# Optimization experiments

Hardware: AMD Instinct MI355X
Metric: run time of the kernel (lower is better)

The kernel has to match this reference:

```python
import jax, jax.numpy as jnp
import numpy as np


def gelu(x):
    # custom GELU classes in such repos typically implement the tanh approximation
    return jax.nn.gelu(x, approximate=True)


def setup_inputs() -> dict:
    key = jax.random.key(0)
    ks = jax.random.split(key, 16)
    B, N1, N2, D, H = 4, 1024, 1024, 256, 4
    prev = jax.random.normal(ks[0], (B, N1, D), dtype=jnp.float32)
    curr = jax.random.normal(ks[1], (B, N2, D), dtype=jnp.float32)
    edges = jax.random.randint(ks[2], (B, N1, N2), 0, 2).astype(jnp.int32)

    def lin(k, fan_in, fan_out):
        kw, kb = jax.random.split(k)
        s = 1.0 / np.sqrt(fan_in)
        W = jax.random.uniform(kw, (fan_in, fan_out), jnp.float32, -s, s)
        b = jax.random.uniform(kb, (fan_out,), jnp.float32, -s, s)
        return W, b

    W_pre, b_pre = lin(ks[3], D, 6)
    W_cur, b_cur = lin(ks[4], D, 6)
    W_fuse, b_fuse = lin(ks[5], 12, 4)
    W_ffn, b_ffn = lin(ks[6], 12, 8)
    W_fcc, b_fcc = lin(ks[7], 8, H)
    W_fcg, b_fcg = lin(ks[8], 8, D)
    return {"prev": prev, "curr": curr, "edges": edges,
            "W_pre": W_pre, "b_pre": b_pre, "W_cur": W_cur, "b_cur": b_cur,
            "W_fuse": W_fuse, "b_fuse": b_fuse, "W_ffn": W_ffn, "b_ffn": b_ffn,
            "W_fcc": W_fcc, "b_fcc": b_fcc, "W_fcg": W_fcg, "b_fcg": b_fcg}


def reference(prev, curr, edges, W_pre, b_pre, W_cur, b_cur,
              W_fuse, b_fuse, W_ffn, b_ffn, W_fcc, b_fcc, W_fcg, b_fcg):
    B, N1, D = prev.shape
    N2 = curr.shape[1]
    H = W_fcc.shape[1]
    Dh = D // H
    mask = edges != 0                                   # [B,N1,N2]

    bt_pre = prev @ W_pre + b_pre                       # [B,N1,6]
    bt_cur = curr @ W_cur + b_cur                       # [B,N2,6]
    pair = jnp.concatenate([
        jnp.broadcast_to(bt_pre[:, :, None, :], (B, N1, N2, 6)),
        jnp.broadcast_to(bt_cur[:, None, :, :], (B, N1, N2, 6))], axis=-1)
    c = gelu(pair) @ W_fuse + b_fuse                    # [B,N1,N2,4]
    c = jnp.where(mask[..., None], c, 0.0)

    e1 = (jnp.sum(edges, axis=1) + 1).astype(c.dtype)   # [B,N2]
    d = jnp.sum(c, axis=1)[:, None] / e1[:, None, :, None]
    d = jnp.broadcast_to(d, c.shape)
    e = jnp.broadcast_to(jnp.max(c, axis=1)[:, None], c.shape)
    fused = gelu(jnp.concatenate([c, d, e], axis=-1)) @ W_ffn + b_ffn  # [B,N1,N2,8]

    att = gelu(fused) @ W_fcc + b_fcc                   # [B,N1,N2,H]
    att = jnp.transpose(att, (0, 2, 1, 3))              # [B,N2,N1,H]
    maskT = jnp.transpose(mask, (0, 2, 1))              # [B,N2,N1]
    logits = jnp.where(maskT[..., None], att, -9e15)
    p = jax.nn.softmax(logits, axis=2)                  # softmax over N1 per head
    p = jnp.where(maskT[..., None], p, 0.0)
    # per-head aggregation: head i uses prev columns [i*Dh, (i+1)*Dh)
    res = jnp.einsum('bmnh,bnhd->bmhd', p, prev.reshape(B, N1, H, Dh)).reshape(B, N2, D)

    fused_m = jnp.where(mask[..., None], fused, 0.0)
    g = jnp.sum(fused_m, axis=1) / e1[..., None]        # [B,N2,8]
    return res + gelu(g) @ W_fcg + b_fcg                # [B,N2,D]
```

## Files before the change

kernel.cpp:

```cpp
#include <hip/hip_runtime.h>


using bf16x8 = __attribute__((ext_vector_type(8))) short;
using f32x4  = __attribute__((ext_vector_type(4))) float;
typedef float v2f __attribute__((ext_vector_type(2)));

__device__ __forceinline__ v2f pk_fma(v2f a, v2f b, v2f c){
    return __builtin_elementwise_fma(a, b, c);
}

__device__ __forceinline__ float gelu_f(float x){
    float x2 = x*x;
    float tt = x * __builtin_fmaf(0.044715f, x2, 1.0f);
    float e  = exp2f(-2.3022082f * tt);
    return x * __builtin_amdgcn_rcpf(1.0f + e);
}

__device__ __forceinline__ v2f gelu2(v2f x){
    v2f x2 = x*x;
    v2f tt = x * pk_fma((v2f){0.044715f,0.044715f}, x2, (v2f){1.0f,1.0f});
    float e0 = exp2f(-2.3022082f * tt[0]);
    float e1 = exp2f(-2.3022082f * tt[1]);
    v2f r = { __builtin_amdgcn_rcpf(1.0f + e0),
              __builtin_amdgcn_rcpf(1.0f + e1) };
    return x * r;
}

__device__ __forceinline__ unsigned short f2bf(float f){
    unsigned int u = __float_as_uint(f);
    u += 0x7FFFu + ((u >> 16) & 1u);
    return (unsigned short)(u >> 16);
}

__global__ __launch_bounds__(256) void k_rowsT(
    const float* __restrict__ prev, const float* __restrict__ curr,
    const float* __restrict__ W_pre, const float* __restrict__ b_pre,
    const float* __restrict__ W_cur, const float* __restrict__ b_cur,
    const float* __restrict__ W_fuse, const float* __restrict__ b_fuse,
    float* __restrict__ u_ws, float* __restrict__ v_ws,
    unsigned short* __restrict__ prevT)
{
    __shared__ float tile[64][65];
    int t = threadIdx.x;
    if (blockIdx.x < 2048){
        int gid  = blockIdx.x * 256 + t;
        int wave = gid >> 6;
        int lane = t & 63;
        bool isPrev = wave < 4096;
        int row = isPrev ? wave : (wave - 4096);
        const float* xrow = (isPrev ? prev : curr) + (size_t)row * 256;
        const float* W  = isPrev ? W_pre : W_cur;
        const float* bv = isPrev ? b_pre : b_cur;

        float4 x4 = *reinterpret_cast<const float4*>(xrow + lane*4);
        const float* Wl = W + lane*24;
        float p[6];
        #pragma unroll
        for (int k=0;k<6;++k)
            p[k] = x4.x*Wl[k] + x4.y*Wl[6+k] + x4.z*Wl[12+k] + x4.w*Wl[18+k];
        #pragma unroll
        for (int off=32; off>=1; off>>=1){
            #pragma unroll
            for (int k=0;k<6;++k) p[k] += __shfl_xor(p[k], off, 64);
        }
        if (lane == 0){
            float g[6];
            #pragma unroll
            for(int k=0;k<6;++k) g[k] = gelu_f(p[k] + bv[k]);
            int rb = isPrev ? 0 : 6;
            float o[4];
            #pragma unroll
            for(int kk=0;kk<4;++kk){
                float a = isPrev ? 0.0f : b_fuse[kk];
                #pragma unroll
                for(int k=0;k<6;++k) a += g[k]*W_fuse[(rb+k)*4+kk];
                o[kk]=a;
            }
            float* dst = (isPrev ? u_ws : v_ws) + (size_t)row*4;
            *reinterpret_cast<float4*>(dst) = make_float4(o[0],o[1],o[2],o[3]);
        }
    } else {
        int pbid = blockIdx.x - 2048;
        int b  = pbid >> 6;
        int it = (pbid >> 2) & 15;
        int dt = pbid & 3;
        int i0 = it*64, d0 = dt*64;
        int col = t & 63, rw = t >> 6;
        #pragma unroll
        for (int r = 0; r < 16; ++r){
            int row = rw + 4*r;
            tile[row][col] = prev[((size_t)b*1024 + i0 + row)*256 + d0 + col];
        }
        __syncthreads();
        #pragma unroll
        for (int r = 0; r < 16; ++r){
            int drow = rw + 4*r;
            prevT[((size_t)b*256 + d0 + drow)*1024 + i0 + col]
                = f2bf(tile[col][drow]);
        }
    }
}

__global__ __launch_bounds__(256) void k_cols(
    const int* __restrict__ edges,
    const float* __restrict__ u_ws, const float* __restrict__ v_ws,
    const float* __restrict__ W_ffn, const float* __restrict__ b_ffn,
    float* __restrict__ Gd_ws, float* __restrict__ cnt_ws)
{
    int b  = blockIdx.x >> 6;
    int j0 = (blockIdx.x & 63) * 16;
    int t  = threadIdx.x;
    int jq = t & 3, sl = t >> 2;
    const int*   eb = edges + (size_t)b*1048576 + j0 + jq*4;
    const float* ub = u_ws + (size_t)b*4096;

    int   cnt[4] = {0,0,0,0};
    float S[4][4] = {{0.f}};
    float M[4][4];
    #pragma unroll
    for (int q=0;q<4;++q)
        #pragma unroll
        for (int k=0;k<4;++k) M[q][k] = -3.4e38f;

    #pragma unroll 4
    for (int ii=0; ii<16; ++ii){
        int i = sl*16 + ii;
        int4   e4 = *reinterpret_cast<const int4*>(eb + (size_t)i*1024);
        float4 u4 = *reinterpret_cast<const float4*>(ub + i*4);
        float uu[4] = {u4.x,u4.y,u4.z,u4.w};
        int   ee[4] = {e4.x,e4.y,e4.z,e4.w};
        #pragma unroll
        for (int q=0;q<4;++q){
            bool mk = ee[q]!=0;
            cnt[q] += mk ? 1 : 0;
            #pragma unroll
            for (int k=0;k<4;++k){
                S[q][k] += mk ? uu[k] : 0.0f;
                M[q][k]  = mk ? fmaxf(M[q][k],uu[k]) : M[q][k];
            }
        }
    }
    __shared__ float rS[64][16][4];
    __shared__ float rM[64][16][4];
    __shared__ int   rC[64][16];
    #pragma unroll
    for (int q=0;q<4;++q){
        int c = jq*4+q;
        #pragma unroll
        for (int k=0;k<4;++k){ rS[sl][c][k]=S[q][k]; rM[sl][c][k]=M[q][k]; }
        rC[sl][c]=cnt[q];
    }
    __syncthreads();
    float aS[4], aM[4]; int aC=0; int c2=0, hf=0;
    if (t < 128){
        c2 = t & 15; hf = t >> 4;
        #pragma unroll
        for(int k=0;k<4;++k){ aS[k]=0.f; aM[k]=-3.4e38f; }
        for (int s2=hf*8; s2<hf*8+8; ++s2){
            aC += rC[s2][c2];
            #pragma unroll
            for(int k=0;k<4;++k){ aS[k]+=rS[s2][c2][k]; aM[k]=fmaxf(aM[k],rM[s2][c2][k]); }
        }
    }
    __syncthreads();
    if (t < 128){
        rC[hf][c2]=aC;
        #pragma unroll
        for(int k=0;k<4;++k){ rS[hf][c2][k]=aS[k]; rM[hf][c2][k]=aM[k]; }
    }
    __syncthreads();
    if (t < 16){
        int cc=0; float Sa[4]={0,0,0,0};
        float Ma[4]={-3.4e38f,-3.4e38f,-3.4e38f,-3.4e38f};
        for (int s2=0;s2<8;++s2){
            cc += rC[s2][t];
            #pragma unroll
            for(int k=0;k<4;++k){ Sa[k]+=rS[s2][t][k]; Ma[k]=fmaxf(Ma[k],rM[s2][t][k]); }
        }
        size_t cj = (size_t)b*1024 + j0 + t;
        float4 v4 = *reinterpret_cast<const float4*>(v_ws + cj*4);
        float vv[4]={v4.x,v4.y,v4.z,v4.w};
        float cf = (float)cc, e1 = cf + 1.0f;
        float gd[4], ge[4];
        #pragma unroll
        for(int k=0;k<4;++k){
            float dk = (Sa[k] + cf*vv[k]) / e1;
            float ek;
            if (cc == 0) ek = 0.0f;
            else { float m1 = Ma[k]+vv[k]; ek = (cc < 1024) ? fmaxf(m1, 0.0f) : m1; }
            gd[k]=gelu_f(dk); ge[k]=gelu_f(ek);
        }
        #pragma unroll
        for(int kk=0;kk<8;++kk){
            float a = b_ffn[kk];
            #pragma unroll
            for(int k=0;k<4;++k)
                a += gd[k]*W_ffn[(4+k)*8+kk] + ge[k]*W_ffn[(8+k)*8+kk];
            Gd_ws[cj*8+kk]=a;
        }
        cnt_ws[cj]=cf;
    }
}

template<int SPLIT>
__global__ __launch_bounds__(256) void k_main(
    const unsigned short* __restrict__ prevT, const int* __restrict__ edges,
    const float* __restrict__ u_ws, const float* __restrict__ v_ws,
    const float* __restrict__ Gd_ws,
    const float* __restrict__ W_ffn, const float* __restrict__ W_fcc,
    const float* __restrict__ b_fcc,
    float* __restrict__ Pws, float* __restrict__ Sws, float* __restrict__ Tws)
{
    const int RPB = 1024/SPLIT;
    int bid = blockIdx.x;
    int sp  = bid & (SPLIT-1);
    int jt  = (bid / SPLIT) & 63;
    int b   = bid / (SPLIT*64);
    int j0  = jt*16;
    int t   = threadIdx.x;
    int lane = t & 63;
    int wv   = t >> 6;
    int jl_w = t & 15, il_w = t >> 4;

    __shared__ unsigned short wA[2][4096];
    __shared__ __align__(16) float sU[2][64][4];
    __shared__ float sV[16][4];
    __shared__ float sGd[16][8];

    if (t < 64)  (&sV[0][0])[t]  = v_ws[((size_t)b*1024 + j0)*4 + t];
    if (t < 128) (&sGd[0][0])[t] = Gd_ws[((size_t)b*1024 + j0)*8 + t];

    const float LOG2E = 1.4426950408889634f;
    v2f W4p[4][4], Wfcp[8][2], bfcp[2];
    #pragma unroll
    for(int k=0;k<4;++k)
        #pragma unroll
        for(int q=0;q<4;++q)
            W4p[k][q] = (v2f){W_ffn[k*8+2*q], W_ffn[k*8+2*q+1]};
    #pragma unroll
    for(int kk=0;kk<8;++kk)
        #pragma unroll
        for(int p2=0;p2<2;++p2)
            Wfcp[kk][p2] = (v2f){W_fcc[kk*4+2*p2]*LOG2E, W_fcc[kk*4+2*p2+1]*LOG2E};
    #pragma unroll
    for(int p2=0;p2<2;++p2)
        bfcp[p2] = (v2f){b_fcc[2*p2]*LOG2E, b_fcc[2*p2+1]*LOG2E};

    f32x4 accm[4];
    #pragma unroll
    for (int tile=0;tile<4;++tile) accm[tile] = (f32x4){0.f,0.f,0.f,0.f};
    f32x4 accs = (f32x4){0.f,0.f,0.f,0.f};
    bf16x8 onesB;
    #pragma unroll
    for (int e=0;e<8;++e) onesB[e] = (short)0x3F80;
    v2f Tp01 = {0,0}, Tp23 = {0,0};

    const int* ebase = edges + (size_t)b*1048576 + j0;
    const int NCH = RPB/64;
    const int base_i0 = sp*RPB;

    int arow = lane & 15, kgrp = lane >> 4;
    int aoff0 = (((wv*16 + arow)*64 + kgrp*8)*2) ^ ((arow & 7) << 4);
    int aoff1 = aoff0 ^ 64;
    const unsigned short* pTbase = prevT
        + ((size_t)b*256 + wv*64 + arow)*1024 + base_i0 + kgrp*8;

    float su_r = u_ws[((size_t)b*1024 + base_i0)*4 + t];
    (&sU[0][0][0])[t] = su_r;
    int egr[4];
    #pragma unroll
    for (int r=0;r<4;++r)
        egr[r] = ebase[(size_t)(base_i0 + il_w + 16*r)*1024 + jl_w];
    {
        int i0n = base_i0 + ((1 < NCH) ? 64 : 0);
        su_r = u_ws[((size_t)b*1024 + i0n)*4 + t];
    }
    __syncthreads();

    float4 v4p = *reinterpret_cast<const float4*>(&sV[jl_w][0]);
    float4 gd0 = *reinterpret_cast<const float4*>(&sGd[jl_w][0]);
    float4 gd1 = *reinterpret_cast<const float4*>(&sGd[jl_w][4]);

    for (int cc=0; cc<NCH; ++cc){
        int p = cc & 1;
        char* wAp = reinterpret_cast<char*>(wA) + p*8192;

        int eg_c[4] = {egr[0], egr[1], egr[2], egr[3]};
        {
            int i0n = base_i0 + ((cc+1 < NCH) ? (cc+1)*64 : 0);
            #pragma unroll
            for (int r=0;r<4;++r)
                egr[r] = ebase[(size_t)(i0n + il_w + 16*r)*1024 + jl_w];
        }

        #pragma unroll
        for (int r=0;r<4;++r){
            int il = il_w + 16*r;
            int eg = eg_c[r];
            float4 u4 = *reinterpret_cast<const float4*>(&sU[p][il][0]);
            v2f g01 = gelu2((v2f){u4.x + v4p.x, u4.y + v4p.y});
            v2f g23 = gelu2((v2f){u4.z + v4p.z, u4.w + v4p.w});
            float m = eg ? 1.0f : 0.0f;
            v2f mm = {m, m};
            Tp01 = pk_fma(mm, g01, Tp01);
            Tp23 = pk_fma(mm, g23, Tp23);
            v2f a0 = {gd0.x, gd0.y}, a1 = {gd0.z, gd0.w};
            v2f a2 = {gd1.x, gd1.y}, a3 = {gd1.z, gd1.w};
            v2f G0 = {g01[0], g01[0]}, G1 = {g01[1], g01[1]};
            v2f G2 = {g23[0], g23[0]}, G3 = {g23[1], g23[1]};
            a0 = pk_fma(G0, W4p[0][0], a0); a1 = pk_fma(G0, W4p[0][1], a1);
            a2 = pk_fma(G0, W4p[0][2], a2); a3 = pk_fma(G0, W4p[0][3], a3);
            a0 = pk_fma(G1, W4p[1][0], a0); a1 = pk_fma(G1, W4p[1][1], a1);
            a2 = pk_fma(G1, W4p[1][2], a2); a3 = pk_fma(G1, W4p[1][3], a3);
            a0 = pk_fma(G2, W4p[2][0], a0); a1 = pk_fma(G2, W4p[2][1], a1);
            a2 = pk_fma(G2, W4p[2][2], a2); a3 = pk_fma(G2, W4p[2][3], a3);
            a0 = pk_fma(G3, W4p[3][0], a0); a1 = pk_fma(G3, W4p[3][1], a1);
            a2 = pk_fma(G3, W4p[3][2], a2); a3 = pk_fma(G3, W4p[3][3], a3);
            v2f f01 = gelu2(a0), f23 = gelu2(a1);
            v2f f45 = gelu2(a2), f67 = gelu2(a3);
            v2f L01 = bfcp[0], L23 = bfcp[1];
            float fv[8] = {f01[0],f01[1],f23[0],f23[1],f45[0],f45[1],f67[0],f67[1]};
            #pragma unroll
            for (int kk=0;kk<8;++kk){
                v2f F = {fv[kk], fv[kk]};
                L01 = pk_fma(F, Wfcp[kk][0], L01);
                L23 = pk_fma(F, Wfcp[kk][1], L23);
            }
            float lg[4] = {L01[0], L01[1], L23[0], L23[1]};
            int low = ((jl_w*64 + il)*2) ^ ((jl_w & 7) << 4);
            #pragma unroll
            for (int hh=0;hh<4;++hh){
                float wf = eg ? exp2f(lg[hh]) : 0.0f;
                *reinterpret_cast<unsigned short*>(wAp + hh*2048 + low) = f2bf(wf);
            }
        }

        (&sU[p^1][0][0])[t] = su_r;
        {
            int i0n2 = base_i0 + ((cc+2 < NCH) ? (cc+2)*64 : 0);
            su_r = u_ws[((size_t)b*1024 + i0n2)*4 + t];
        }
        __syncthreads();

        bf16x8 afr0 = *reinterpret_cast<const bf16x8*>(wAp + aoff0);
        bf16x8 afr1 = *reinterpret_cast<const bf16x8*>(wAp + aoff1);
        const unsigned short* pT = pTbase + (size_t)cc*64;
        #pragma unroll
        for (int tile=0; tile<4; ++tile){
            const unsigned short* pB = pT + (size_t)tile*16*1024;
            bf16x8 bfr0 = *reinterpret_cast<const bf16x8*>(pB);
            bf16x8 bfr1 = *reinterpret_cast<const bf16x8*>(pB + 32);
            accm[tile] = __builtin_amdgcn_mfma_f32_16x16x32_bf16(
                afr0, bfr0, accm[tile], 0, 0, 0);
            accm[tile] = __builtin_amdgcn_mfma_f32_16x16x32_bf16(
                afr1, bfr1, accm[tile], 0, 0, 0);
        }
        accs = __builtin_amdgcn_mfma_f32_16x16x32_bf16(afr0, onesB, accs, 0,0,0);
        accs = __builtin_amdgcn_mfma_f32_16x16x32_bf16(afr1, onesB, accs, 0,0,0);
    }

    size_t bp = ((size_t)b*64 + jt)*SPLIT + sp;

    float* sT4 = reinterpret_cast<float*>(wA);
    {
        float* ts = sT4 + (size_t)t*4;
        ts[0]=Tp01[0]; ts[1]=Tp01[1]; ts[2]=Tp23[0]; ts[3]=Tp23[1];
    }
    __syncthreads();
    if (t < 16){
        float T0=0,T1=0,T2=0,T3=0;
        for (int s2=0;s2<16;++s2){
            const float* p = sT4 + (size_t)(s2*16 + t)*4;
            T0+=p[0]; T1+=p[1]; T2+=p[2]; T3+=p[3];
        }
        float* td = Tws + (bp*16 + t)*4;
        td[0]=T0; td[1]=T1; td[2]=T2; td[3]=T3;
    }

    if (arow == 0){
        #pragma unroll
        for (int r2=0; r2<4; ++r2)
            Sws[bp*64 + wv*16 + kgrp*4 + r2] = accs[r2];
    }
    {
        #pragma unroll
        for (int tile=0; tile<4; ++tile){
            #pragma unroll
            for (int r2=0; r2<4; ++r2){
                int j   = kgrp*4 + r2;
                int dim = wv*64 + tile*16 + arow;
                Pws[((size_t)bp*16 + j)*256 + dim] = accm[tile][r2];
            }
        }
    }
}

template<int SPLIT>
__global__ __launch_bounds__(256) void k_merge(
    const float* __restrict__ Pws, const float* __restrict__ Sws,
    const float* __restrict__ Tws,
    const float* __restrict__ Gd_ws, const float* __restrict__ cnt_ws,
    const float* __restrict__ W_ffn, const float* __restrict__ W_fcg,
    const float* __restrict__ b_fcg, float* __restrict__ out)
{
    int b   = blockIdx.x >> 7;
    int jt8 = blockIdx.x & 127;
    int jt16 = jt8 >> 1;
    int cb  = (jt8 & 1) * 8;
    int j0  = jt8*8;
    int t  = threadIdx.x;
    int jl = t >> 5, hd = t & 31, h = hd >> 3, dq = hd & 7;
    int col = cb + jl;
    __shared__ float sG[8][8];

    size_t bp0 = ((size_t)b*64 + jt16)*SPLIT;
    float s = 0.0f, acc[8] = {0,0,0,0,0,0,0,0};
    #pragma unroll
    for (int sp2=0; sp2<SPLIT; ++sp2){
        const float* p = Pws + ((bp0+sp2)*16 + col)*256 + hd*8;
        float4 p0 = *reinterpret_cast<const float4*>(p);
        float4 p1 = *reinterpret_cast<const float4*>(p+4);
        acc[0]+=p0.x; acc[1]+=p0.y; acc[2]+=p0.z; acc[3]+=p0.w;
        acc[4]+=p1.x; acc[5]+=p1.y; acc[6]+=p1.z; acc[7]+=p1.w;
        s += Sws[(bp0+sp2)*64 + h*16 + col];
    }
    if (t < 8){
        float T[4] = {0,0,0,0};
        #pragma unroll
        for (int sp2=0; sp2<SPLIT; ++sp2){
            const float* tp = Tws + ((bp0+sp2)*16 + cb + t)*4;
            #pragma unroll
            for (int k=0;k<4;++k) T[k]+=tp[k];
        }
        size_t cj = (size_t)b*1024 + j0 + t;
        float cf = cnt_ws[cj];
        float inv = __fdividef(1.0f, cf + 1.0f);
        #pragma unroll
        for (int kk=0;kk<8;++kk){
            float a = cf*Gd_ws[cj*8+kk];
            #pragma unroll
            for (int k=0;k<4;++k) a += T[k]*W_ffn[k*8+kk];
            sG[t][kk] = gelu_f(a*inv);
        }
    }
    __syncthreads();

    float rs = (s > 0.0f) ? (1.0f/s) : 0.0f;
    int col0 = h*64 + dq*8;
    float gg[8];
    #pragma unroll
    for (int kk=0;kk<8;++kk) gg[kk]=sG[jl][kk];
    float o[8];
    #pragma unroll
    for (int d2=0;d2<8;++d2){
        float a = b_fcg[col0+d2];
        #pragma unroll
        for (int kk=0;kk<8;++kk) a += gg[kk]*W_fcg[kk*256 + col0 + d2];
        o[d2] = acc[d2]*rs + a;
    }
    float* ob = out + ((size_t)b*1024 + j0 + jl)*256 + col0;
    float4* o4 = reinterpret_cast<float4*>(ob);
    o4[0] = make_float4(o[0],o[1],o[2],o[3]);
    o4[1] = make_float4(o[4],o[5],o[6],o[7]);
}

extern "C" void kernel_launch(void* const* d_in, const int* in_sizes, int n_in,
                              void* d_out, int out_size, void* d_ws, size_t ws_size,
                              hipStream_t stream)
{
    const float* prev  = (const float*)d_in[0];
    const float* curr  = (const float*)d_in[1];
    const int*   edges = (const int*)  d_in[2];
    const float* W_pre = (const float*)d_in[3];
    const float* b_pre = (const float*)d_in[4];
    const float* W_cur = (const float*)d_in[5];
    const float* b_cur = (const float*)d_in[6];
    const float* W_fuse= (const float*)d_in[7];
    const float* b_fuse= (const float*)d_in[8];
    const float* W_ffn = (const float*)d_in[9];
    const float* b_ffn = (const float*)d_in[10];
    const float* W_fcc = (const float*)d_in[11];
    const float* b_fcc = (const float*)d_in[12];
    const float* W_fcg = (const float*)d_in[13];
    const float* b_fcg = (const float*)d_in[14];
    float* out = (float*)d_out;

    float* u_ws   = (float*)d_ws;
    float* v_ws   = u_ws  + 16384;
    float* Gd_ws  = v_ws  + 16384;
    float* cnt_ws = Gd_ws + 32768;
    float* Pws    = cnt_ws + 4096;
    const size_t base_f = 16384 + 16384 + 32768 + 4096;

    const size_t p4  = (size_t)1024*16*256;
    const size_t s4v = (size_t)1024*64;
    const size_t t4  = (size_t)1024*16*4;
    const size_t pT_f = (size_t)4*256*1024/2;
    const size_t need4 = (base_f + p4 + s4v + t4 + pT_f) * 4;
    const size_t p2 = p4/2, s2v = s4v/2, t2 = t4/2;
    const size_t need2 = (base_f + p2 + s2v + t2 + pT_f) * 4;
    const size_t p1 = p4/4, s1 = s4v/4, t1 = t4/4;

    if (ws_size >= need4){
        float* Sws = Pws + p4;
        float* Tws = Sws + s4v;
        unsigned short* prevT = (unsigned short*)(Tws + t4);
        k_rowsT<<<dim3(2304), dim3(256), 0, stream>>>(prev, curr, W_pre, b_pre,
            W_cur, b_cur, W_fuse, b_fuse, u_ws, v_ws, prevT);
        k_cols<<<dim3(256), dim3(256), 0, stream>>>(edges, u_ws, v_ws,
            W_ffn, b_ffn, Gd_ws, cnt_ws);
        k_main<4><<<dim3(1024), dim3(256), 0, stream>>>(prevT, edges, u_ws,
            v_ws, Gd_ws, W_ffn, W_fcc, b_fcc, Pws, Sws, Tws);
        k_merge<4><<<dim3(512), dim3(256), 0, stream>>>(Pws, Sws, Tws, Gd_ws,
            cnt_ws, W_ffn, W_fcg, b_fcg, out);
    } else if (ws_size >= need2){
        float* Sws = Pws + p2;
        float* Tws = Sws + s2v;
        unsigned short* prevT = (unsigned short*)(Tws + t2);
        k_rowsT<<<dim3(2304), dim3(256), 0, stream>>>(prev, curr, W_pre, b_pre,
            W_cur, b_cur, W_fuse, b_fuse, u_ws, v_ws, prevT);
        k_cols<<<dim3(256), dim3(256), 0, stream>>>(edges, u_ws, v_ws,
            W_ffn, b_ffn, Gd_ws, cnt_ws);
        k_main<2><<<dim3(512), dim3(256), 0, stream>>>(prevT, edges, u_ws,
            v_ws, Gd_ws, W_ffn, W_fcc, b_fcc, Pws, Sws, Tws);
        k_merge<2><<<dim3(512), dim3(256), 0, stream>>>(Pws, Sws, Tws, Gd_ws,
            cnt_ws, W_ffn, W_fcg, b_fcg, out);
    } else {
        float* Sws = Pws + p1;
        float* Tws = Sws + s1;
        unsigned short* prevT = (unsigned short*)(Tws + t1);
        k_rowsT<<<dim3(2304), dim3(256), 0, stream>>>(prev, curr, W_pre, b_pre,
            W_cur, b_cur, W_fuse, b_fuse, u_ws, v_ws, prevT);
        k_cols<<<dim3(256), dim3(256), 0, stream>>>(edges, u_ws, v_ws,
            W_ffn, b_ffn, Gd_ws, cnt_ws);
        k_main<1><<<dim3(256), dim3(256), 0, stream>>>(prevT, edges, u_ws,
            v_ws, Gd_ws, W_ffn, W_fcc, b_fcc, Pws, Sws, Tws);
        k_merge<1><<<dim3(512), dim3(256), 0, stream>>>(Pws, Sws, Tws, Gd_ws,
            cnt_ws, W_ffn, W_fcg, b_fcg, out);
    }
}
```

Measured before the change: 69.61 us.

## Split main kernel's reduction rows eight ways and single-buffer shared staging

Adds an eight-way split over the N1 reduction dimension of the main attention kernel, which doubles the grid to 2048 blocks, when the workspace is large enough. The shared-memory double buffers for the weight tile and u rows become single buffers, with an extra barrier per chunk. The aim is more parallelism and lower LDS use per block, so occupancy can rise. The cost is more partial results for the merge kernel to reduce, half as many chunks per block, and an added sync point that serialises the staging step. The SPLIT=1 fallback path is removed.

```diff
diff --git a/kernel.cpp b/kernel.cpp
--- a/kernel.cpp
+++ b/kernel.cpp
@@ -222,8 +222,8 @@
     int wv   = t >> 6;
     int jl_w = t & 15, il_w = t >> 4;
 
-    __shared__ unsigned short wA[2][4096];
-    __shared__ __align__(16) float sU[2][64][4];
+    __shared__ unsigned short wA[4096];
+    __shared__ __align__(16) float sU[64][4];
     __shared__ float sV[16][4];
     __shared__ float sGd[16][8];
 
@@ -266,15 +266,10 @@
         + ((size_t)b*256 + wv*64 + arow)*1024 + base_i0 + kgrp*8;
 
     float su_r = u_ws[((size_t)b*1024 + base_i0)*4 + t];
-    (&sU[0][0][0])[t] = su_r;
     int egr[4];
     #pragma unroll
     for (int r=0;r<4;++r)
         egr[r] = ebase[(size_t)(base_i0 + il_w + 16*r)*1024 + jl_w];
-    {
-        int i0n = base_i0 + ((1 < NCH) ? 64 : 0);
-        su_r = u_ws[((size_t)b*1024 + i0n)*4 + t];
-    }
     __syncthreads();
 
     float4 v4p = *reinterpret_cast<const float4*>(&sV[jl_w][0]);
@@ -282,12 +277,13 @@
     float4 gd1 = *reinterpret_cast<const float4*>(&sGd[jl_w][4]);
 
     for (int cc=0; cc<NCH; ++cc){
-        int p = cc & 1;
-        char* wAp = reinterpret_cast<char*>(wA) + p*8192;
+        (&sU[0][0])[t] = su_r;
+        __syncthreads();
 
         int eg_c[4] = {egr[0], egr[1], egr[2], egr[3]};
         {
             int i0n = base_i0 + ((cc+1 < NCH) ? (cc+1)*64 : 0);
+            su_r = u_ws[((size_t)b*1024 + i0n)*4 + t];
             #pragma unroll
             for (int r=0;r<4;++r)
                 egr[r] = ebase[(size_t)(i0n + il_w + 16*r)*1024 + jl_w];
@@ -297,7 +293,7 @@
         for (int r=0;r<4;++r){
             int il = il_w + 16*r;
             int eg = eg_c[r];
-            float4 u4 = *reinterpret_cast<const float4*>(&sU[p][il][0]);
+            float4 u4 = *reinterpret_cast<const float4*>(&sU[il][0]);
             v2f g01 = gelu2((v2f){u4.x + v4p.x, u4.y + v4p.y});
             v2f g23 = gelu2((v2f){u4.z + v4p.z, u4.w + v4p.w});
             float m = eg ? 1.0f : 0.0f;
@@ -331,19 +327,16 @@
             #pragma unroll
             for (int hh=0;hh<4;++hh){
                 float wf = eg ? exp2f(lg[hh]) : 0.0f;
-                *reinterpret_cast<unsigned short*>(wAp + hh*2048 + low) = f2bf(wf);
+                *reinterpret_cast<unsigned short*>(
+                    reinterpret_cast<char*>(wA) + hh*2048 + low) = f2bf(wf);
             }
         }
-
-        (&sU[p^1][0][0])[t] = su_r;
-        {
-            int i0n2 = base_i0 + ((cc+2 < NCH) ? (cc+2)*64 : 0);
-            su_r = u_ws[((size_t)b*1024 + i0n2)*4 + t];
-        }
         __syncthreads();
 
-        bf16x8 afr0 = *reinterpret_cast<const bf16x8*>(wAp + aoff0);
-        bf16x8 afr1 = *reinterpret_cast<const bf16x8*>(wAp + aoff1);
+        bf16x8 afr0 = *reinterpret_cast<const bf16x8*>(
+            reinterpret_cast<const char*>(wA) + aoff0);
+        bf16x8 afr1 = *reinterpret_cast<const bf16x8*>(
+            reinterpret_cast<const char*>(wA) + aoff1);
         const unsigned short* pT = pTbase + (size_t)cc*64;
         #pragma unroll
         for (int tile=0; tile<4; ++tile){
@@ -361,6 +354,7 @@
 
     size_t bp = ((size_t)b*64 + jt)*SPLIT + sp;
 
+    __syncthreads();
     float* sT4 = reinterpret_cast<float*>(wA);
     {
         float* ts = sT4 + (size_t)t*4;
@@ -492,16 +486,28 @@
     float* Pws    = cnt_ws + 4096;
     const size_t base_f = 16384 + 16384 + 32768 + 4096;
 
-    const size_t p4  = (size_t)1024*16*256;
-    const size_t s4v = (size_t)1024*64;
-    const size_t t4  = (size_t)1024*16*4;
+    const size_t p8  = (size_t)2048*16*256;
+    const size_t s8  = (size_t)2048*64;
+    const size_t t8  = (size_t)2048*16*4;
     const size_t pT_f = (size_t)4*256*1024/2;
+    const size_t need8 = (base_f + p8 + s8 + t8 + pT_f) * 4;
+    const size_t p4 = p8/2, s4v = s8/2, t4 = t8/2;
     const size_t need4 = (base_f + p4 + s4v + t4 + pT_f) * 4;
-    const size_t p2 = p4/2, s2v = s4v/2, t2 = t4/2;
-    const size_t need2 = (base_f + p2 + s2v + t2 + pT_f) * 4;
-    const size_t p1 = p4/4, s1 = s4v/4, t1 = t4/4;
-
-    if (ws_size >= need4){
+    const size_t p2 = p8/4, s2v = s8/4, t2 = t8/4;
+
+    if (ws_size >= need8){
+        float* Sws = Pws + p8;
+        float* Tws = Sws + s8;
+        unsigned short* prevT = (unsigned short*)(Tws + t8);
+        k_rowsT<<<dim3(2304), dim3(256), 0, stream>>>(prev, curr, W_pre, b_pre,
+            W_cur, b_cur, W_fuse, b_fuse, u_ws, v_ws, prevT);
+        k_cols<<<dim3(256), dim3(256), 0, stream>>>(edges, u_ws, v_ws,
+            W_ffn, b_ffn, Gd_ws, cnt_ws);
+        k_main<8><<<dim3(2048), dim3(256), 0, stream>>>(prevT, edges, u_ws,
+            v_ws, Gd_ws, W_ffn, W_fcc, b_fcc, Pws, Sws, Tws);
+        k_merge<8><<<dim3(512), dim3(256), 0, stream>>>(Pws, Sws, Tws, Gd_ws,
+            cnt_ws, W_ffn, W_fcg, b_fcg, out);
+    } else if (ws_size >= need4){
         float* Sws = Pws + p4;
         float* Tws = Sws + s4v;
         unsigned short* prevT = (unsigned short*)(Tws + t4);
@@ -513,7 +519,7 @@
             v_ws, Gd_ws, W_ffn, W_fcc, b_fcc, Pws, Sws, Tws);
         k_merge<4><<<dim3(512), dim3(256), 0, stream>>>(Pws, Sws, Tws, Gd_ws,
             cnt_ws, W_ffn, W_fcg, b_fcg, out);
-    } else if (ws_size >= need2){
+    } else {
         float* Sws = Pws + p2;
         float* Tws = Sws + s2v;
         unsigned short* prevT = (unsigned short*)(Tws + t2);
@@ -525,17 +531,5 @@
             v_ws, Gd_ws, W_ffn, W_fcc, b_fcc, Pws, Sws, Tws);
         k_merge<2><<<dim3(512), dim3(256), 0, stream>>>(Pws, Sws, Tws, Gd_ws,
             cnt_ws, W_ffn, W_fcg, b_fcg, out);
-    } else {
-        float* Sws = Pws + p1;
-        float* Tws = Sws + s1;
-        unsigned short* prevT = (unsigned short*)(Tws + t1);
-        k_rowsT<<<dim3(2304), dim3(256), 0, stream>>>(prev, curr, W_pre, b_pre,
-            W_cur, b_cur, W_fuse, b_fuse, u_ws, v_ws, prevT);
-        k_cols<<<dim3(256), dim3(256), 0, stream>>>(edges, u_ws, v_ws,
-            W_ffn, b_ffn, Gd_ws, cnt_ws);
-        k_main<1><<<dim3(256), dim3(256), 0, stream>>>(prevT, edges, u_ws,
-            v_ws, Gd_ws, W_ffn, W_fcc, b_fcc, Pws, Sws, Tws);
-        k_merge<1><<<dim3(512), dim3(256), 0, stream>>>(Pws, Sws, Tws, Gd_ws,
-            cnt_ws, W_ffn, W_fcg, b_fcg, out);
-    }
-}
+    }
+}
```

Result: faster. 64.91 us (-6.7%).
